# Performance work log

Hardware: AMD Instinct MI355X
Metric: run time of the kernel (lower is better)

The kernel has to match this reference:

```python
import jax, jax.numpy as jnp
import numpy as np

EMBED_DIM = 1024
NUM_HEADS = 16
HEAD_DIM = EMBED_DIM // NUM_HEADS
WINDOW = 256
B, S = 2, 2048


def setup_inputs() -> dict:
    key = jax.random.key(0)
    ks = jax.random.split(key, 9)
    sc = 1.0 / np.sqrt(EMBED_DIM)
    inp = {
        "x": jax.random.normal(ks[0], (B, S, EMBED_DIM), dtype=jnp.float32),
        "Wq": jax.random.normal(ks[1], (EMBED_DIM, EMBED_DIM), dtype=jnp.float32) * sc,
        "Wk": jax.random.normal(ks[2], (EMBED_DIM, EMBED_DIM), dtype=jnp.float32) * sc,
        "Wv": jax.random.normal(ks[3], (EMBED_DIM, EMBED_DIM), dtype=jnp.float32) * sc,
        "Wo": jax.random.normal(ks[4], (EMBED_DIM, EMBED_DIM), dtype=jnp.float32) * sc,
        "bq": jax.random.normal(ks[5], (EMBED_DIM,), dtype=jnp.float32) * 0.01,
        "bk": jax.random.normal(ks[6], (EMBED_DIM,), dtype=jnp.float32) * 0.01,
        "bv": jax.random.normal(ks[7], (EMBED_DIM,), dtype=jnp.float32) * 0.01,
        "bo": jax.random.normal(ks[8], (EMBED_DIM,), dtype=jnp.float32) * 0.01,
    }
    return inp


def _sliding_window_mask(seq_len: int) -> jnp.ndarray:
    # True where attention is NOT permitted (future or beyond window)
    idx = jnp.arange(seq_len)
    rel = idx[None, :] - idx[:, None]  # (S, S): key_pos - query_pos
    return (rel > 0) | (rel < -WINDOW)


def reference(x, Wq, Wk, Wv, Wo, bq, bk, bv, bo):
    Bx, Sx, E = x.shape
    H, D = NUM_HEADS, HEAD_DIM
    # projections (torch Linear: y = x @ W.T + b)
    q = (x @ Wq.T + bq).reshape(Bx, Sx, H, D).transpose(0, 2, 1, 3)  # (B,H,S,D)
    k = (x @ Wk.T + bk).reshape(Bx, Sx, H, D).transpose(0, 2, 1, 3)
    v = (x @ Wv.T + bv).reshape(Bx, Sx, H, D).transpose(0, 2, 1, 3)
    q = q * (D ** -0.5)
    attn = jnp.einsum("bhqd,bhkd->bhqk", q, k)  # (B,H,S,S) dense scores
    mask = _sliding_window_mask(Sx)
    attn = jnp.where(mask, -jnp.inf, attn)
    attn = jax.nn.softmax(attn, axis=-1)
    y = jnp.einsum("bhqk,bhkd->bhqd", attn, v)
    y = y.transpose(0, 2, 1, 3).reshape(Bx, Sx, E)
    return y @ Wo.T + bo
```

## Files before the change

kernel.cpp:

```cpp
#include <hip/hip_runtime.h>

#define E_DIM 1024
#define NHEAD 16
#define HDIM 64
#define SEQ 2048
#define NBATCH 2
#define WIN 256
#define MTOK (NBATCH * SEQ)
#define BKT 32
#define NT (E_DIM / BKT)

typedef __attribute__((ext_vector_type(4))) float f32x4;
typedef __attribute__((ext_vector_type(8))) short short8;
typedef __attribute__((ext_vector_type(4))) unsigned short u16x4;

#define AS1 __attribute__((address_space(1)))
#define AS3 __attribute__((address_space(3)))

__device__ __forceinline__ void gll16(const void* g, void* l) {
    __builtin_amdgcn_global_load_lds((const AS1 void*)g, (AS3 void*)l, 16, 0, 0);
}

__device__ __forceinline__ unsigned short f2bf(float f) {
    union { float f; unsigned u; } a; a.f = f;
    unsigned r = a.u + 0x7fffu + ((a.u >> 16) & 1u);
    return (unsigned short)(r >> 16);
}

__global__ __launch_bounds__(256) void conv_all(const float* __restrict__ x,
        const float* __restrict__ w0, const float* __restrict__ w1,
        const float* __restrict__ w2, const float* __restrict__ w3,
        unsigned short* __restrict__ xo,
        unsigned short* __restrict__ o0, unsigned short* __restrict__ o1,
        unsigned short* __restrict__ o2, unsigned short* __restrict__ o3) {
    const int seg = blockIdx.y;
    const float* src;
    unsigned short* dst;
    if (seg < 4) { src = x + (size_t)seg * 1048576; dst = xo + (size_t)seg * 1048576; }
    else {
        src = (seg == 4) ? w0 : (seg == 5) ? w1 : (seg == 6) ? w2 : w3;
        dst = (seg == 4) ? o0 : (seg == 5) ? o1 : (seg == 6) ? o2 : o3;
    }
    int i = blockIdx.x * 256 + threadIdx.x;
    float4 v = ((const float4*)src)[i];
    u16x4 o;
    o[0] = f2bf(v.x); o[1] = f2bf(v.y); o[2] = f2bf(v.z); o[3] = f2bf(v.w);
    ((u16x4*)dst)[i] = o;
}

__global__ __launch_bounds__(512, 2) void gemm8_qkv(const unsigned short* __restrict__ xb,
        const unsigned short* __restrict__ wqb, const unsigned short* __restrict__ wkb,
        const unsigned short* __restrict__ wvb,
        const float* __restrict__ bq, const float* __restrict__ bk, const float* __restrict__ bv,
        unsigned short* __restrict__ qo, unsigned short* __restrict__ ko,
        unsigned short* __restrict__ vTo) {
    __shared__ char lds[131072];
    const int tid = threadIdx.x;
    const int w = tid >> 6, l = tid & 63;
    const int r16 = l & 15, kq = l >> 4;
    const int wm = w >> 2, wn = w & 3;
    const int m0 = blockIdx.x * 256;
    const int by = blockIdx.y;
    const int mat = by >> 2;
    const int nb = (by & 3) * 256;
    const unsigned short* Bw = (mat == 0) ? wqb : (mat == 1) ? wkb : wvb;

    const int srow = tid >> 2;
    const int sslot = tid & 3;
    const int fsw = (srow >> 1) & 3;
    const int gslot = (sslot ^ fsw) * 8;
    const unsigned short* aSrc0 = xb + (size_t)(m0 + srow) * E_DIM + gslot;
    const unsigned short* aSrc1 = aSrc0 + (size_t)128 * E_DIM;
    const unsigned short* bSrc0 = Bw + (size_t)(nb + srow) * E_DIM + gslot;
    const unsigned short* bSrc1 = bSrc0 + (size_t)128 * E_DIM;
    const int dstOff = w * 1024;

#define STAGE_A(t) { char* d_ = lds + ((t) & 3) * 32768 + dstOff; \
                     gll16(aSrc0 + (t) * BKT, d_); gll16(aSrc1 + (t) * BKT, d_ + 8192); }
#define STAGE_B(t) { char* d_ = lds + ((t) & 3) * 32768 + 16384 + dstOff; \
                     gll16(bSrc0 + (t) * BKT, d_); gll16(bSrc1 + (t) * BKT, d_ + 8192); }

    f32x4 acc[8][4];
    #pragma unroll
    for (int m = 0; m < 8; ++m)
        #pragma unroll
        for (int n = 0; n < 4; ++n)
            acc[m][n] = (f32x4){0.f, 0.f, 0.f, 0.f};

    STAGE_A(0); STAGE_B(0); STAGE_A(1); STAGE_B(1);

    const int fs = (r16 >> 1) & 3;
    const int rdoff = (kq ^ fs) * 16;

    for (int t = 0; t < NT; ++t) {
        if (t < NT - 1) { asm volatile("s_waitcnt vmcnt(4)" ::: "memory"); }
        else            { asm volatile("s_waitcnt vmcnt(0)" ::: "memory"); }
        __builtin_amdgcn_sched_barrier(0);
        __builtin_amdgcn_s_barrier();
        __builtin_amdgcn_sched_barrier(0);
        char* la = lds + (t & 3) * 32768;
        char* lb = la + 16384;
        short8 bfr[4], af[8];
        #pragma unroll
        for (int n = 0; n < 4; ++n)
            bfr[n] = *(const short8*)(lb + (wn * 64 + n * 16 + r16) * 64 + rdoff);
        #pragma unroll
        for (int j = 0; j < 8; ++j)
            af[j] = *(const short8*)(la + (wm * 128 + j * 16 + r16) * 64 + rdoff);
        if (t + 2 < NT) { STAGE_A(t + 2); STAGE_B(t + 2); }
        __builtin_amdgcn_s_setprio(1);
        #pragma unroll
        for (int j = 0; j < 8; ++j)
            #pragma unroll
            for (int n = 0; n < 4; ++n)
                acc[j][n] = __builtin_amdgcn_mfma_f32_16x16x32_bf16(af[j], bfr[n], acc[j][n], 0, 0, 0);
        __builtin_amdgcn_s_setprio(0);
    }
#undef STAGE_A
#undef STAGE_B

    const float* bias = (mat == 0) ? bq : (mat == 1) ? bk : bv;
    const float scale = (mat == 0) ? 0.125f : 1.0f;
    #pragma unroll
    for (int n = 0; n < 4; ++n) {
        int e = nb + wn * 64 + n * 16 + r16;
        float bb = bias[e];
        int h = e >> 6, d = e & 63;
        #pragma unroll
        for (int m = 0; m < 8; ++m) {
            int tok = m0 + wm * 128 + m * 16 + kq * 4;
            int b = tok >> 11, s = tok & (SEQ - 1);
            if (mat == 2) {
                u16x4 o;
                #pragma unroll
                for (int r = 0; r < 4; ++r) o[r] = f2bf(acc[m][n][r] + bb);
                *(u16x4*)(vTo + ((size_t)(b * NHEAD + h) * HDIM + d) * SEQ + s) = o;
            } else {
                unsigned short* dst = (mat == 0) ? qo : ko;
                #pragma unroll
                for (int r = 0; r < 4; ++r) {
                    float val = (acc[m][n][r] + bb) * scale;
                    dst[((size_t)(b * NHEAD + h) * SEQ + s + r) * HDIM + d] = f2bf(val);
                }
            }
        }
    }
}

__global__ __launch_bounds__(256, 2) void gemm_out(const unsigned short* __restrict__ yb,
        const unsigned short* __restrict__ wob, const float* __restrict__ bo,
        float* __restrict__ out) {
    __shared__ char lds[65536];
    const int tid = threadIdx.x;
    const int w = tid >> 6, l = tid & 63;
    const int r16 = l & 15, kq = l >> 4;
    const int wr = w >> 1, wc = w & 1;
    const int m0 = blockIdx.x * 128;
    const int n0 = blockIdx.y * 128;

    const int srow = tid >> 2;
    const int sslot = tid & 3;
    const int fsw = (srow >> 1) & 3;
    const int gslot = (sslot ^ fsw) * 8;
    const unsigned short* aSrc0 = yb + (size_t)(m0 + srow) * E_DIM + gslot;
    const unsigned short* aSrc1 = aSrc0 + (size_t)64 * E_DIM;
    const unsigned short* bSrc0 = wob + (size_t)(n0 + srow) * E_DIM + gslot;
    const unsigned short* bSrc1 = bSrc0 + (size_t)64 * E_DIM;
    const int dstOff = w * 1024;

#define STAGE_A(t) { char* d_ = lds + ((t) & 3) * 16384 + dstOff; \
                     gll16(aSrc0 + (t) * BKT, d_); gll16(aSrc1 + (t) * BKT, d_ + 4096); }
#define STAGE_B(t) { char* d_ = lds + ((t) & 3) * 16384 + 8192 + dstOff; \
                     gll16(bSrc0 + (t) * BKT, d_); gll16(bSrc1 + (t) * BKT, d_ + 4096); }

    f32x4 acc[4][4];
    #pragma unroll
    for (int m = 0; m < 4; ++m)
        #pragma unroll
        for (int n = 0; n < 4; ++n)
            acc[m][n] = (f32x4){0.f, 0.f, 0.f, 0.f};

    STAGE_A(0); STAGE_B(0); STAGE_A(1); STAGE_B(1);

    const int fs = (r16 >> 1) & 3;
    const int rdoff = (kq ^ fs) * 16;

    for (int t = 0; t < NT; ++t) {
        if (t < NT - 1) { asm volatile("s_waitcnt vmcnt(4)" ::: "memory"); }
        else            { asm volatile("s_waitcnt vmcnt(0)" ::: "memory"); }
        __builtin_amdgcn_sched_barrier(0);
        __builtin_amdgcn_s_barrier();
        __builtin_amdgcn_sched_barrier(0);
        char* la = lds + (t & 3) * 16384;
        char* lb = la + 8192;
        short8 bfr[4], af[4];
        #pragma unroll
        for (int n = 0; n < 4; ++n)
            bfr[n] = *(const short8*)(lb + (wc * 64 + n * 16 + r16) * 64 + rdoff);
        #pragma unroll
        for (int m = 0; m < 4; ++m)
            af[m] = *(const short8*)(la + (wr * 64 + m * 16 + r16) * 64 + rdoff);
        if (t + 2 < NT) { STAGE_A(t + 2); STAGE_B(t + 2); }
        __builtin_amdgcn_s_setprio(1);
        #pragma unroll
        for (int m = 0; m < 4; ++m)
            #pragma unroll
            for (int n = 0; n < 4; ++n)
                acc[m][n] = __builtin_amdgcn_mfma_f32_16x16x32_bf16(af[m], bfr[n], acc[m][n], 0, 0, 0);
        __builtin_amdgcn_s_setprio(0);
    }
#undef STAGE_A
#undef STAGE_B

    #pragma unroll
    for (int n = 0; n < 4; ++n) {
        int e = n0 + wc * 64 + n * 16 + r16;
        float bb = bo[e];
        #pragma unroll
        for (int m = 0; m < 4; ++m) {
            #pragma unroll
            for (int r = 0; r < 4; ++r) {
                int tok = m0 + wr * 64 + m * 16 + kq * 4 + r;
                out[(size_t)tok * E_DIM + e] = acc[m][n][r] + bb;
            }
        }
    }
}

__global__ __launch_bounds__(256) void attn_swa(const unsigned short* __restrict__ q,
                                                const unsigned short* __restrict__ k,
                                                const unsigned short* __restrict__ vT,
                                                unsigned short* __restrict__ y) {
    __shared__ char plds[4 * 4096];
    const int t = threadIdx.x;
    const int w = t >> 6, l = t & 63;
    const int r16 = l & 15, kq = l >> 4;
    const int wid = blockIdx.x * 4 + w;
    const int bh = wid >> 6;
    const int q0 = (wid & 63) * 32;
    const unsigned short* qp = q + (size_t)bh * SEQ * HDIM;
    const unsigned short* kp = k + (size_t)bh * SEQ * HDIM;
    const unsigned short* vp = vT + (size_t)bh * HDIM * SEQ;
    char* pl = plds + w * 4096;

    short8 qf[2][2];
    #pragma unroll
    for (int mf = 0; mf < 2; ++mf) {
        const unsigned short* qr = qp + (q0 + mf * 16 + r16) * HDIM + kq * 8;
        qf[mf][0] = *(const short8*)(qr);
        qf[mf][1] = *(const short8*)(qr + 32);
    }

    f32x4 po[2][4];
    float mrow[2][4], lrow[2][4];
    #pragma unroll
    for (int mf = 0; mf < 2; ++mf) {
        #pragma unroll
        for (int nn = 0; nn < 4; ++nn) po[mf][nn] = (f32x4){0.f, 0.f, 0.f, 0.f};
        #pragma unroll
        for (int r = 0; r < 4; ++r) { mrow[mf][r] = -1e30f; lrow[mf][r] = 0.f; }
    }

    const int kstart = (q0 >= WIN) ? (q0 - WIN) : 0;
    for (int k0 = kstart; k0 <= q0 + 31; k0 += 32) {
        short8 kf[2][2];
        #pragma unroll
        for (int n = 0; n < 2; ++n) {
            const unsigned short* kr = kp + (size_t)(k0 + n * 16 + r16) * HDIM + kq * 8;
            kf[n][0] = *(const short8*)(kr);
            kf[n][1] = *(const short8*)(kr + 32);
        }
        f32x4 sc[2][2];
        #pragma unroll
        for (int mf = 0; mf < 2; ++mf)
            #pragma unroll
            for (int n = 0; n < 2; ++n) {
                f32x4 z = {0.f, 0.f, 0.f, 0.f};
                z = __builtin_amdgcn_mfma_f32_16x16x32_bf16(qf[mf][0], kf[n][0], z, 0, 0, 0);
                sc[mf][n] = __builtin_amdgcn_mfma_f32_16x16x32_bf16(qf[mf][1], kf[n][1], z, 0, 0, 0);
            }
        float tmax[2][4];
        #pragma unroll
        for (int mf = 0; mf < 2; ++mf)
            #pragma unroll
            for (int r = 0; r < 4; ++r) {
                int qrow = q0 + mf * 16 + kq * 4 + r;
                int key0 = k0 + r16;
                int key1 = key0 + 16;
                if (!(key0 <= qrow && key0 >= qrow - WIN)) sc[mf][0][r] = -1e30f;
                if (!(key1 <= qrow && key1 >= qrow - WIN)) sc[mf][1][r] = -1e30f;
                tmax[mf][r] = fmaxf(sc[mf][0][r], sc[mf][1][r]);
            }
        #pragma unroll
        for (int off = 1; off < 16; off <<= 1)
            #pragma unroll
            for (int mf = 0; mf < 2; ++mf)
                #pragma unroll
                for (int r = 0; r < 4; ++r)
                    tmax[mf][r] = fmaxf(tmax[mf][r], __shfl_xor(tmax[mf][r], off));
        float pv[2][2][4], psum[2][4];
        #pragma unroll
        for (int mf = 0; mf < 2; ++mf)
            #pragma unroll
            for (int r = 0; r < 4; ++r) {
                float mnew = fmaxf(mrow[mf][r], tmax[mf][r]);
                float resc = __expf(mrow[mf][r] - mnew);
                mrow[mf][r] = mnew;
                lrow[mf][r] *= resc;
                po[mf][0][r] *= resc; po[mf][1][r] *= resc;
                po[mf][2][r] *= resc; po[mf][3][r] *= resc;
                float p0 = (sc[mf][0][r] > -1e29f) ? __expf(sc[mf][0][r] - mnew) : 0.f;
                float p1 = (sc[mf][1][r] > -1e29f) ? __expf(sc[mf][1][r] - mnew) : 0.f;
                pv[mf][0][r] = p0; pv[mf][1][r] = p1;
                psum[mf][r] = p0 + p1;
            }
        #pragma unroll
        for (int off = 1; off < 16; off <<= 1)
            #pragma unroll
            for (int mf = 0; mf < 2; ++mf)
                #pragma unroll
                for (int r = 0; r < 4; ++r)
                    psum[mf][r] += __shfl_xor(psum[mf][r], off);
        #pragma unroll
        for (int mf = 0; mf < 2; ++mf)
            #pragma unroll
            for (int r = 0; r < 4; ++r) lrow[mf][r] += psum[mf][r];

        #pragma unroll
        for (int mf = 0; mf < 2; ++mf)
            #pragma unroll
            for (int r = 0; r < 4; ++r) {
                int row = kq * 4 + r;
                int c0 = r16 ^ ((row & 7) << 3);
                int c1 = (16 + r16) ^ ((row & 7) << 3);
                *(unsigned short*)(pl + mf * 2048 + row * 128 + c0 * 2) = f2bf(pv[mf][0][r]);
                *(unsigned short*)(pl + mf * 2048 + row * 128 + c1 * 2) = f2bf(pv[mf][1][r]);
            }
        short8 pa[2];
        #pragma unroll
        for (int mf = 0; mf < 2; ++mf)
            pa[mf] = *(const short8*)(pl + mf * 2048 + r16 * 128 + ((kq ^ (r16 & 7)) * 16));
        #pragma unroll
        for (int nn = 0; nn < 4; ++nn) {
            short8 vf = *(const short8*)(vp + (size_t)(nn * 16 + r16) * SEQ + k0 + kq * 8);
            po[0][nn] = __builtin_amdgcn_mfma_f32_16x16x32_bf16(pa[0], vf, po[0][nn], 0, 0, 0);
            po[1][nn] = __builtin_amdgcn_mfma_f32_16x16x32_bf16(pa[1], vf, po[1][nn], 0, 0, 0);
        }
    }

    const int b = bh >> 4, h = bh & 15;
    #pragma unroll
    for (int mf = 0; mf < 2; ++mf)
        #pragma unroll
        for (int nn = 0; nn < 4; ++nn)
            #pragma unroll
            for (int r = 0; r < 4; ++r) {
                int s = q0 + mf * 16 + kq * 4 + r;
                float val = po[mf][nn][r] / lrow[mf][r];
                y[((size_t)(b * SEQ + s)) * E_DIM + h * HDIM + nn * 16 + r16] = f2bf(val);
            }
}

extern "C" void kernel_launch(void* const* d_in, const int* in_sizes, int n_in,
                              void* d_out, int out_size, void* d_ws, size_t ws_size,
                              hipStream_t stream) {
    const float* x  = (const float*)d_in[0];
    const float* Wq = (const float*)d_in[1];
    const float* Wk = (const float*)d_in[2];
    const float* Wv = (const float*)d_in[3];
    const float* Wo = (const float*)d_in[4];
    const float* bq = (const float*)d_in[5];
    const float* bk = (const float*)d_in[6];
    const float* bv = (const float*)d_in[7];
    const float* bo = (const float*)d_in[8];
    float* out = (float*)d_out;

    char* ws = (char*)d_ws;
    unsigned short* xb  = (unsigned short*)(ws);
    unsigned short* wqb = (unsigned short*)(ws + ((size_t)8 << 20));
    unsigned short* wkb = (unsigned short*)(ws + ((size_t)10 << 20));
    unsigned short* wvb = (unsigned short*)(ws + ((size_t)12 << 20));
    unsigned short* wob = (unsigned short*)(ws + ((size_t)14 << 20));
    unsigned short* qw  = (unsigned short*)(ws + ((size_t)16 << 20));
    unsigned short* kw  = (unsigned short*)(ws + ((size_t)24 << 20));
    unsigned short* vTw = (unsigned short*)(ws + ((size_t)40 << 20));
    unsigned short* yw  = (unsigned short*)(ws + ((size_t)48 << 20));

    conv_all<<<dim3(1024, 8), 256, 0, stream>>>(x, Wq, Wk, Wv, Wo, xb, wqb, wkb, wvb, wob);

    gemm8_qkv<<<dim3(16, 12), 512, 0, stream>>>(xb, wqb, wkb, wvb, bq, bk, bv, qw, kw, vTw);
    attn_swa<<<512, 256, 0, stream>>>(qw, kw, vTw, yw);
    gemm_out<<<dim3(32, 8), 256, 0, stream>>>(yw, wob, bo, out);
}
```

Baseline: 166.1 us.

## Split attention loop into masked edge and unmasked interior tiles with K prefetch

Restructures the sliding-window attention inner loop into a templated tile function. Masking applies only to the first (window edge) and last (diagonal) tiles, and interior tiles skip the mask checks. The next K tile and the current V fragments are loaded early to overlap memory latency with compute. The per-tile cross-lane row-sum shuffle is replaced by per-lane partial sums reduced once at the end, at the cost of extra registers for prefetched fragments.

```diff
diff --git a/kernel.cpp b/kernel.cpp
--- a/kernel.cpp
+++ b/kernel.cpp
@@ -227,6 +227,93 @@
     }
 }
 
+template<int MODE, bool PRE>
+__device__ __forceinline__ void attn_tile(int k0,
+        const unsigned short* __restrict__ kp, const unsigned short* __restrict__ vp,
+        int r16, int kq, char* pl,
+        const short8 (&qf)[2][2], short8 (&kf)[2][2],
+        f32x4 (&po)[2][4], float (&mrow)[2][4], float (&lsum)[2][4]) {
+    f32x4 sc[2][2];
+    #pragma unroll
+    for (int mf = 0; mf < 2; ++mf)
+        #pragma unroll
+        for (int n = 0; n < 2; ++n) {
+            f32x4 z = {0.f, 0.f, 0.f, 0.f};
+            z = __builtin_amdgcn_mfma_f32_16x16x32_bf16(qf[mf][0], kf[n][0], z, 0, 0, 0);
+            sc[mf][n] = __builtin_amdgcn_mfma_f32_16x16x32_bf16(qf[mf][1], kf[n][1], z, 0, 0, 0);
+        }
+    if (PRE) {
+        #pragma unroll
+        for (int n = 0; n < 2; ++n) {
+            const unsigned short* kr = kp + (size_t)(k0 + 32 + n * 16 + r16) * HDIM + kq * 8;
+            kf[n][0] = *(const short8*)(kr);
+            kf[n][1] = *(const short8*)(kr + 32);
+        }
+    }
+    short8 vf[4];
+    #pragma unroll
+    for (int nn = 0; nn < 4; ++nn)
+        vf[nn] = *(const short8*)(vp + (size_t)(nn * 16 + r16) * SEQ + k0 + kq * 8);
+
+    float tmax[2][4];
+    #pragma unroll
+    for (int mf = 0; mf < 2; ++mf)
+        #pragma unroll
+        for (int r = 0; r < 4; ++r) {
+            int rel = mf * 16 + kq * 4 + r;
+            if (MODE == 1) {
+                if (r16 < rel)      sc[mf][0][r] = -1e30f;
+                if (16 + r16 < rel) sc[mf][1][r] = -1e30f;
+            }
+            if (MODE == 2) {
+                if (r16 > rel)      sc[mf][0][r] = -1e30f;
+                if (16 + r16 > rel) sc[mf][1][r] = -1e30f;
+            }
+            tmax[mf][r] = fmaxf(sc[mf][0][r], sc[mf][1][r]);
+        }
+    #pragma unroll
+    for (int off = 1; off < 16; off <<= 1)
+        #pragma unroll
+        for (int mf = 0; mf < 2; ++mf)
+            #pragma unroll
+            for (int r = 0; r < 4; ++r)
+                tmax[mf][r] = fmaxf(tmax[mf][r], __shfl_xor(tmax[mf][r], off));
+    float pv[2][2][4];
+    #pragma unroll
+    for (int mf = 0; mf < 2; ++mf)
+        #pragma unroll
+        for (int r = 0; r < 4; ++r) {
+            float mnew = fmaxf(mrow[mf][r], tmax[mf][r]);
+            float resc = __expf(mrow[mf][r] - mnew);
+            mrow[mf][r] = mnew;
+            float p0 = __expf(sc[mf][0][r] - mnew);
+            float p1 = __expf(sc[mf][1][r] - mnew);
+            lsum[mf][r] = lsum[mf][r] * resc + p0 + p1;
+            po[mf][0][r] *= resc; po[mf][1][r] *= resc;
+            po[mf][2][r] *= resc; po[mf][3][r] *= resc;
+            pv[mf][0][r] = p0; pv[mf][1][r] = p1;
+        }
+    #pragma unroll
+    for (int mf = 0; mf < 2; ++mf)
+        #pragma unroll
+        for (int r = 0; r < 4; ++r) {
+            int row = kq * 4 + r;
+            int c0 = r16 ^ ((row & 7) << 3);
+            int c1 = c0 ^ 16;
+            *(unsigned short*)(pl + mf * 2048 + row * 128 + c0 * 2) = f2bf(pv[mf][0][r]);
+            *(unsigned short*)(pl + mf * 2048 + row * 128 + c1 * 2) = f2bf(pv[mf][1][r]);
+        }
+    short8 pa[2];
+    #pragma unroll
+    for (int mf = 0; mf < 2; ++mf)
+        pa[mf] = *(const short8*)(pl + mf * 2048 + r16 * 128 + ((kq ^ (r16 & 7)) * 16));
+    #pragma unroll
+    for (int nn = 0; nn < 4; ++nn) {
+        po[0][nn] = __builtin_amdgcn_mfma_f32_16x16x32_bf16(pa[0], vf[nn], po[0][nn], 0, 0, 0);
+        po[1][nn] = __builtin_amdgcn_mfma_f32_16x16x32_bf16(pa[1], vf[nn], po[1][nn], 0, 0, 0);
+    }
+}
+
 __global__ __launch_bounds__(256) void attn_swa(const unsigned short* __restrict__ q,
                                                 const unsigned short* __restrict__ k,
                                                 const unsigned short* __restrict__ vT,
@@ -252,101 +339,40 @@
     }
 
     f32x4 po[2][4];
-    float mrow[2][4], lrow[2][4];
+    float mrow[2][4], lsum[2][4];
     #pragma unroll
     for (int mf = 0; mf < 2; ++mf) {
         #pragma unroll
         for (int nn = 0; nn < 4; ++nn) po[mf][nn] = (f32x4){0.f, 0.f, 0.f, 0.f};
         #pragma unroll
-        for (int r = 0; r < 4; ++r) { mrow[mf][r] = -1e30f; lrow[mf][r] = 0.f; }
+        for (int r = 0; r < 4; ++r) { mrow[mf][r] = -1e30f; lsum[mf][r] = 0.f; }
     }
 
     const int kstart = (q0 >= WIN) ? (q0 - WIN) : 0;
-    for (int k0 = kstart; k0 <= q0 + 31; k0 += 32) {
-        short8 kf[2][2];
-        #pragma unroll
-        for (int n = 0; n < 2; ++n) {
-            const unsigned short* kr = kp + (size_t)(k0 + n * 16 + r16) * HDIM + kq * 8;
-            kf[n][0] = *(const short8*)(kr);
-            kf[n][1] = *(const short8*)(kr + 32);
-        }
-        f32x4 sc[2][2];
+    short8 kf[2][2];
+    #pragma unroll
+    for (int n = 0; n < 2; ++n) {
+        const unsigned short* kr = kp + (size_t)(kstart + n * 16 + r16) * HDIM + kq * 8;
+        kf[n][0] = *(const short8*)(kr);
+        kf[n][1] = *(const short8*)(kr + 32);
+    }
+
+    int k0 = kstart;
+    if (q0 >= WIN) {
+        attn_tile<1, true>(k0, kp, vp, r16, kq, pl, qf, kf, po, mrow, lsum);
+        k0 += 32;
+    }
+    for (; k0 < q0; k0 += 32)
+        attn_tile<0, true>(k0, kp, vp, r16, kq, pl, qf, kf, po, mrow, lsum);
+    attn_tile<2, false>(q0, kp, vp, r16, kq, pl, qf, kf, po, mrow, lsum);
+
+    #pragma unroll
+    for (int off = 1; off < 16; off <<= 1)
         #pragma unroll
         for (int mf = 0; mf < 2; ++mf)
             #pragma unroll
-            for (int n = 0; n < 2; ++n) {
-                f32x4 z = {0.f, 0.f, 0.f, 0.f};
-                z = __builtin_amdgcn_mfma_f32_16x16x32_bf16(qf[mf][0], kf[n][0], z, 0, 0, 0);
-                sc[mf][n] = __builtin_amdgcn_mfma_f32_16x16x32_bf16(qf[mf][1], kf[n][1], z, 0, 0, 0);
-            }
-        float tmax[2][4];
-        #pragma unroll
-        for (int mf = 0; mf < 2; ++mf)
-            #pragma unroll
-            for (int r = 0; r < 4; ++r) {
-                int qrow = q0 + mf * 16 + kq * 4 + r;
-                int key0 = k0 + r16;
-                int key1 = key0 + 16;
-                if (!(key0 <= qrow && key0 >= qrow - WIN)) sc[mf][0][r] = -1e30f;
-                if (!(key1 <= qrow && key1 >= qrow - WIN)) sc[mf][1][r] = -1e30f;
-                tmax[mf][r] = fmaxf(sc[mf][0][r], sc[mf][1][r]);
-            }
-        #pragma unroll
-        for (int off = 1; off < 16; off <<= 1)
-            #pragma unroll
-            for (int mf = 0; mf < 2; ++mf)
-                #pragma unroll
-                for (int r = 0; r < 4; ++r)
-                    tmax[mf][r] = fmaxf(tmax[mf][r], __shfl_xor(tmax[mf][r], off));
-        float pv[2][2][4], psum[2][4];
-        #pragma unroll
-        for (int mf = 0; mf < 2; ++mf)
-            #pragma unroll
-            for (int r = 0; r < 4; ++r) {
-                float mnew = fmaxf(mrow[mf][r], tmax[mf][r]);
-                float resc = __expf(mrow[mf][r] - mnew);
-                mrow[mf][r] = mnew;
-                lrow[mf][r] *= resc;
-                po[mf][0][r] *= resc; po[mf][1][r] *= resc;
-                po[mf][2][r] *= resc; po[mf][3][r] *= resc;
-                float p0 = (sc[mf][0][r] > -1e29f) ? __expf(sc[mf][0][r] - mnew) : 0.f;
-                float p1 = (sc[mf][1][r] > -1e29f) ? __expf(sc[mf][1][r] - mnew) : 0.f;
-                pv[mf][0][r] = p0; pv[mf][1][r] = p1;
-                psum[mf][r] = p0 + p1;
-            }
-        #pragma unroll
-        for (int off = 1; off < 16; off <<= 1)
-            #pragma unroll
-            for (int mf = 0; mf < 2; ++mf)
-                #pragma unroll
-                for (int r = 0; r < 4; ++r)
-                    psum[mf][r] += __shfl_xor(psum[mf][r], off);
-        #pragma unroll
-        for (int mf = 0; mf < 2; ++mf)
-            #pragma unroll
-            for (int r = 0; r < 4; ++r) lrow[mf][r] += psum[mf][r];
-
-        #pragma unroll
-        for (int mf = 0; mf < 2; ++mf)
-            #pragma unroll
-            for (int r = 0; r < 4; ++r) {
-                int row = kq * 4 + r;
-                int c0 = r16 ^ ((row & 7) << 3);
-                int c1 = (16 + r16) ^ ((row & 7) << 3);
-                *(unsigned short*)(pl + mf * 2048 + row * 128 + c0 * 2) = f2bf(pv[mf][0][r]);
-                *(unsigned short*)(pl + mf * 2048 + row * 128 + c1 * 2) = f2bf(pv[mf][1][r]);
-            }
-        short8 pa[2];
-        #pragma unroll
-        for (int mf = 0; mf < 2; ++mf)
-            pa[mf] = *(const short8*)(pl + mf * 2048 + r16 * 128 + ((kq ^ (r16 & 7)) * 16));
-        #pragma unroll
-        for (int nn = 0; nn < 4; ++nn) {
-            short8 vf = *(const short8*)(vp + (size_t)(nn * 16 + r16) * SEQ + k0 + kq * 8);
-            po[0][nn] = __builtin_amdgcn_mfma_f32_16x16x32_bf16(pa[0], vf, po[0][nn], 0, 0, 0);
-            po[1][nn] = __builtin_amdgcn_mfma_f32_16x16x32_bf16(pa[1], vf, po[1][nn], 0, 0, 0);
-        }
-    }
+            for (int r = 0; r < 4; ++r)
+                lsum[mf][r] += __shfl_xor(lsum[mf][r], off);
 
     const int b = bh >> 4, h = bh & 15;
     #pragma unroll
@@ -356,7 +382,7 @@
             #pragma unroll
             for (int r = 0; r < 4; ++r) {
                 int s = q0 + mf * 16 + kq * 4 + r;
-                float val = po[mf][nn][r] / lrow[mf][r];
+                float val = po[mf][nn][r] / lsum[mf][r];
                 y[((size_t)(b * SEQ + s)) * E_DIM + h * HDIM + nn * 16 + r16] = f2bf(val);
             }
 }
```

New measurement: 162.2 us. 2.3% less time.
